# Kernel tuning notes

Hardware: AMD Instinct MI355X
Metric: run time of the kernel (lower is better)

## Reference

```python
import jax, jax.numpy as jnp
import numpy as np

NUM_HEADS = 8
LN_EPS = 1e-5


def _layernorm(x, g, b):
    m = jnp.mean(x, axis=-1, keepdims=True)
    v = jnp.mean(jnp.square(x - m), axis=-1, keepdims=True)
    return (x - m) * jax.lax.rsqrt(v + LN_EPS) * g + b


def setup_inputs() -> dict:
    key = jax.random.key(0)
    ks = jax.random.split(key, 10)
    D, C, Cin = 2, 256, 64  # depth, embed dim, input channels
    w = lambda k, shape: jax.random.normal(k, shape, jnp.float32) * 0.02
    return {
        "x": jax.random.normal(ks[0], (4, Cin, 12, 12, 12), jnp.float32),
        "W_pe": w(ks[1], (Cin, C)),
        "b_pe": jnp.zeros((C,), jnp.float32),
        "cls_token": w(ks[2], (1, 1, C)),
        "ln1_g": jnp.ones((D, C), jnp.float32),
        "ln1_b": jnp.zeros((D, C), jnp.float32),
        "Wqkv": w(ks[3], (D, C, 3 * C)),
        "Wproj": w(ks[4], (D, C, C)),
        "bproj": jnp.zeros((D, C), jnp.float32),
        "ln2_g": jnp.ones((D, C), jnp.float32),
        "ln2_b": jnp.zeros((D, C), jnp.float32),
        "W1": w(ks[5], (D, C, C)),
        "b1": jnp.zeros((D, C), jnp.float32),
        "W2": w(ks[6], (D, C, C)),
        "b2": jnp.zeros((D, C), jnp.float32),
        "normf_g": jnp.ones((C,), jnp.float32),
        "normf_b": jnp.zeros((C,), jnp.float32),
    }


def reference(x, W_pe, b_pe, cls_token, ln1_g, ln1_b, Wqkv, Wproj, bproj,
              ln2_g, ln2_b, W1, b1, W2, b2, normf_g, normf_b):
    B, Cin, H, W, L = x.shape
    C = W_pe.shape[1]
    hd = C // NUM_HEADS
    scale = hd ** (-0.5)

    # PatchEmbed: 1x1x1 Conv3d == per-voxel linear projection, then flatten to tokens
    tok = jnp.einsum('bchwl,cd->bhwld', x, W_pe).reshape(B, H * W * L, C) + b_pe
    cls = jnp.broadcast_to(cls_token, (B, 1, C))
    t = jnp.concatenate([cls, tok], axis=1)  # [B, N, C], N = H*W*L + 1
    N = t.shape[1]

    depth = Wqkv.shape[0]
    for i in range(depth):
        # --- self-attention ---
        y = _layernorm(t, ln1_g[i], ln1_b[i])
        qkv = (y @ Wqkv[i]).reshape(B, N, 3, NUM_HEADS, hd)
        qkv = jnp.transpose(qkv, (2, 0, 3, 1, 4))  # [3, B, H, N, hd]
        q, k, v = qkv[0], qkv[1], qkv[2]
        attn = jnp.einsum('bhnd,bhmd->bhnm', q, k) * scale
        attn = jax.nn.softmax(attn, axis=-1)
        o = jnp.einsum('bhnm,bhmd->bhnd', attn, v)
        o = jnp.transpose(o, (0, 2, 1, 3)).reshape(B, N, C)
        t = t + (o @ Wproj[i] + bproj[i])
        # --- MLP (mlp_ratio=1.0, exact GELU) ---
        y = _layernorm(t, ln2_g[i], ln2_b[i])
        h = jax.nn.gelu(y @ W1[i] + b1[i], approximate=False)
        t = t + (h @ W2[i] + b2[i])

    t = _layernorm(t, normf_g, normf_b)
    x_cls = t[:, 0]                                   # [B, C]
    feat = t[:, 1:]                                   # [B, H*W*L, C]
    feat = jnp.transpose(feat, (0, 2, 1)).reshape(B, C, H, W, L)  # downsample = Identity for dim=256
    return x_cls, feat
```

## Files before the change

### kernel.cpp

```cpp
#include <hip/hip_runtime.h>
#include <hip/hip_bf16.h>
#include <math.h>

#define B_   4
#define CIN  64
#define P_   1728
#define N_   1729
#define C_   256
#define NH_  8
#define HD_  32
#define M_   (B_*N_)
#define NPAD 1792

typedef __bf16 bf16x8 __attribute__((ext_vector_type(8)));
typedef __bf16 bf16x4 __attribute__((ext_vector_type(4)));
typedef float  f32x4  __attribute__((ext_vector_type(4)));

__global__ __launch_bounds__(256) void embed2(
    const float* __restrict__ x, const float* __restrict__ Wpe,
    const float* __restrict__ bpe, const float* __restrict__ cls,
    float* __restrict__ t)
{
    int idx = blockIdx.x*256 + threadIdx.x;
    int c   = idx & 255;
    int n   = (idx >> 8) % N_;
    int b   = idx / (N_*256);
    if (n == 0) { t[idx] = cls[c]; return; }
    int p = n - 1;
    float acc = bpe[c];
    for (int ci = 0; ci < CIN; ++ci)
        acc += x[(size_t)(b*CIN + ci)*P_ + p] * Wpe[ci*C_ + c];
    t[idx] = acc;
}

__global__ __launch_bounds__(256) void ln4(
    const float* __restrict__ in, __bf16* __restrict__ out,
    const float* __restrict__ g, const float* __restrict__ bb)
{
    int wv = threadIdx.x >> 6, lane = threadIdx.x & 63;
    size_t row = (size_t)blockIdx.x*4 + wv;
    float4 v = *(const float4*)&in[row*C_ + lane*4];
    float s1 = (v.x+v.y)+(v.z+v.w);
    float s2 = (v.x*v.x+v.y*v.y)+(v.z*v.z+v.w*v.w);
    #pragma unroll
    for (int off = 32; off >= 1; off >>= 1) {
        s1 += __shfl_xor(s1, off);
        s2 += __shfl_xor(s2, off);
    }
    float mean = s1*(1.0f/C_);
    float var  = fmaxf(s2*(1.0f/C_) - mean*mean, 0.0f);
    float rstd = rsqrtf(var + 1e-5f);
    float4 gg = *(const float4*)&g[lane*4];
    float4 bv = *(const float4*)&bb[lane*4];
    bf16x4 r;
    r[0] = (__bf16)((v.x-mean)*rstd*gg.x + bv.x);
    r[1] = (__bf16)((v.y-mean)*rstd*gg.y + bv.y);
    r[2] = (__bf16)((v.z-mean)*rstd*gg.z + bv.z);
    r[3] = (__bf16)((v.w-mean)*rstd*gg.w + bv.w);
    *(bf16x4*)&out[row*C_ + lane*4] = r;
}

__global__ __launch_bounds__(256) void ln4f(
    const float* __restrict__ in, float* __restrict__ out,
    const float* __restrict__ g, const float* __restrict__ bb,
    float* __restrict__ cls_out)
{
    int wv = threadIdx.x >> 6, lane = threadIdx.x & 63;
    size_t row = (size_t)blockIdx.x*4 + wv;
    float4 v = *(const float4*)&in[row*C_ + lane*4];
    float s1 = (v.x+v.y)+(v.z+v.w);
    float s2 = (v.x*v.x+v.y*v.y)+(v.z*v.z+v.w*v.w);
    #pragma unroll
    for (int off = 32; off >= 1; off >>= 1) {
        s1 += __shfl_xor(s1, off);
        s2 += __shfl_xor(s2, off);
    }
    float mean = s1*(1.0f/C_);
    float var  = fmaxf(s2*(1.0f/C_) - mean*mean, 0.0f);
    float rstd = rsqrtf(var + 1e-5f);
    float4 gg = *(const float4*)&g[lane*4];
    float4 bv = *(const float4*)&bb[lane*4];
    float4 r;
    r.x = (v.x-mean)*rstd*gg.x + bv.x;
    r.y = (v.y-mean)*rstd*gg.y + bv.y;
    r.z = (v.z-mean)*rstd*gg.z + bv.z;
    r.w = (v.w-mean)*rstd*gg.w + bv.w;
    *(float4*)&out[row*C_ + lane*4] = r;
    if ((row % N_) == 0)
        *(float4*)&cls_out[(row / N_)*C_ + lane*4] = r;
}

__global__ __launch_bounds__(256) void wprep2(
    const float* __restrict__ Wqkv, const float* __restrict__ Wproj,
    const float* __restrict__ W1,   const float* __restrict__ W2,
    __bf16* __restrict__ wT)
{
    int z = blockIdx.z, which = z >> 1, layer = z & 1;
    const float* src; __bf16* dst; int NC;
    if (which == 0) {
        src = Wqkv + (size_t)layer*C_*768;
        dst = wT   + (size_t)layer*768*256;
        NC  = 768;
    } else {
        NC = 256;
        const float* b3 = (which == 1) ? Wproj : (which == 2) ? W1 : W2;
        src = b3 + (size_t)layer*65536;
        dst = wT + 2*768*256 + (size_t)((which-1)*2 + layer)*65536;
    }
    int n0 = blockIdx.x*32; if (n0 >= NC) return;
    int k0 = blockIdx.y*32;
    __shared__ float tile[32][33];
    int c = threadIdx.x & 31, r = threadIdx.x >> 5;
    for (int rr = r; rr < 32; rr += 8)
        tile[rr][c] = src[(size_t)(k0+rr)*NC + n0 + c];
    __syncthreads();
    for (int rr = r; rr < 32; rr += 8)
        dst[(size_t)(n0+rr)*256 + k0 + c] = (__bf16)tile[c][rr];
}

__global__ __launch_bounds__(256) void padzero(
    __bf16* __restrict__ kB, __bf16* __restrict__ vB)
{
    int idx = blockIdx.x*256 + threadIdx.x;
    if (idx >= 32*63*32) return;
    int d  = idx & 31;
    int n  = (idx >> 5) % 63 + N_;
    int bh = idx / (63*32);
    kB[((size_t)bh*NPAD + n)*32 + d] = (__bf16)0.f;
    vB[((size_t)bh*32 + d)*NPAD + n] = (__bf16)0.f;
}

template<int NC, bool ADD, bool GELU, bool BIAS, bool OUTBF>
__global__ __launch_bounds__(256) void gemm3(
    const __bf16* __restrict__ A, const __bf16* __restrict__ Wt,
    const float* __restrict__ bias, float* __restrict__ outF,
    __bf16* __restrict__ outB)
{
    __shared__ __align__(16) __bf16 As[64*64];
    __shared__ __align__(16) __bf16 Bs[64*64];
    int r0 = blockIdx.x*64, c0 = blockIdx.y*64;
    int tid = threadIdx.x;
    int wv = tid >> 6, lane = tid & 63, quad = lane >> 4, mn = lane & 15;
    int sr = tid >> 2, sc = tid & 3;
    int ga = r0 + sr; if (ga >= M_) ga = M_ - 1;

    f32x4 acc[4];
    #pragma unroll
    for (int ct = 0; ct < 4; ++ct)
        #pragma unroll
        for (int rr = 0; rr < 4; ++rr) acc[ct][rr] = 0.f;

    for (int kc = 0; kc < 4; ++kc) {
        __syncthreads();
        *(bf16x8*)&As[sr*64 + ((sc ^ (sr & 7))*8)] =
            *(const bf16x8*)&A[(size_t)ga*256 + kc*64 + sc*8];
        *(bf16x8*)&As[sr*64 + (((sc+4) ^ (sr & 7))*8)] =
            *(const bf16x8*)&A[(size_t)ga*256 + kc*64 + sc*8 + 32];
        *(bf16x8*)&Bs[sr*64 + ((sc ^ (sr & 7))*8)] =
            *(const bf16x8*)&Wt[(size_t)(c0+sr)*256 + kc*64 + sc*8];
        *(bf16x8*)&Bs[sr*64 + (((sc+4) ^ (sr & 7))*8)] =
            *(const bf16x8*)&Wt[(size_t)(c0+sr)*256 + kc*64 + sc*8 + 32];
        __syncthreads();

        #pragma unroll
        for (int h = 0; h < 2; ++h) {
            bf16x8 a = *(const bf16x8*)&As[(wv*16 + mn)*64 + (((h*4+quad) ^ (mn & 7))*8)];
            #pragma unroll
            for (int ct = 0; ct < 4; ++ct) {
                bf16x8 b = *(const bf16x8*)&Bs[(ct*16 + mn)*64 + (((h*4+quad) ^ (mn & 7))*8)];
                acc[ct] = __builtin_amdgcn_mfma_f32_16x16x32_bf16(a, b, acc[ct], 0, 0, 0);
            }
        }
    }

    #pragma unroll
    for (int ct = 0; ct < 4; ++ct) {
        int col = c0 + ct*16 + mn;
        #pragma unroll
        for (int rr = 0; rr < 4; ++rr) {
            int row = r0 + wv*16 + quad*4 + rr;
            if (row >= M_) continue;
            float val = acc[ct][rr];
            if (BIAS) val += bias[col];
            if (GELU) val = 0.5f*val*(1.f + erff(val*0.70710678118654752f));
            size_t oi = (size_t)row*NC + col;
            if (OUTBF) outB[oi] = (__bf16)val;
            else if (ADD) outF[oi] += val;
            else outF[oi] = val;
        }
    }
}

__global__ __launch_bounds__(256) void gemm_qkv3(
    const __bf16* __restrict__ A, const __bf16* __restrict__ Wt,
    __bf16* __restrict__ qB, __bf16* __restrict__ kB, __bf16* __restrict__ vB)
{
    __shared__ __align__(16) __bf16 As[64*64];
    __shared__ __align__(16) __bf16 Bs[64*64];
    int r0 = blockIdx.x*64, c0 = blockIdx.y*64;
    int tid = threadIdx.x;
    int wv = tid >> 6, lane = tid & 63, quad = lane >> 4, mn = lane & 15;
    int sr = tid >> 2, sc = tid & 3;
    int ga = r0 + sr; if (ga >= M_) ga = M_ - 1;

    f32x4 acc[4];
    #pragma unroll
    for (int ct = 0; ct < 4; ++ct)
        #pragma unroll
        for (int rr = 0; rr < 4; ++rr) acc[ct][rr] = 0.f;

    for (int kc = 0; kc < 4; ++kc) {
        __syncthreads();
        *(bf16x8*)&As[sr*64 + ((sc ^ (sr & 7))*8)] =
            *(const bf16x8*)&A[(size_t)ga*256 + kc*64 + sc*8];
        *(bf16x8*)&As[sr*64 + (((sc+4) ^ (sr & 7))*8)] =
            *(const bf16x8*)&A[(size_t)ga*256 + kc*64 + sc*8 + 32];
        *(bf16x8*)&Bs[sr*64 + ((sc ^ (sr & 7))*8)] =
            *(const bf16x8*)&Wt[(size_t)(c0+sr)*256 + kc*64 + sc*8];
        *(bf16x8*)&Bs[sr*64 + (((sc+4) ^ (sr & 7))*8)] =
            *(const bf16x8*)&Wt[(size_t)(c0+sr)*256 + kc*64 + sc*8 + 32];
        __syncthreads();

        #pragma unroll
        for (int h = 0; h < 2; ++h) {
            bf16x8 a = *(const bf16x8*)&As[(wv*16 + mn)*64 + (((h*4+quad) ^ (mn & 7))*8)];
            #pragma unroll
            for (int ct = 0; ct < 4; ++ct) {
                bf16x8 b = *(const bf16x8*)&Bs[(ct*16 + mn)*64 + (((h*4+quad) ^ (mn & 7))*8)];
                acc[ct] = __builtin_amdgcn_mfma_f32_16x16x32_bf16(a, b, acc[ct], 0, 0, 0);
            }
        }
    }

    const float scale = 0.17677669529663687f;
    #pragma unroll
    for (int ct = 0; ct < 4; ++ct) {
        int col = c0 + ct*16 + mn;
        #pragma unroll
        for (int rr = 0; rr < 4; ++rr) {
            int row = r0 + wv*16 + quad*4 + rr;
            if (row >= M_) continue;
            int b = row / N_, n = row - b*N_;
            float val = acc[ct][rr];
            if (col < 256) {
                int h = col >> 5, dd = col & 31;
                qB[((size_t)(b*NH_+h)*NPAD + n)*32 + dd] = (__bf16)(val*scale);
            } else if (col < 512) {
                int h = (col-256) >> 5, dd = col & 31;
                kB[((size_t)(b*NH_+h)*NPAD + n)*32 + dd] = (__bf16)val;
            } else {
                int h = (col-512) >> 5, dd = col & 31;
                vB[((size_t)(b*NH_+h)*32 + dd)*NPAD + n] = (__bf16)val;
            }
        }
    }
}

__global__ __launch_bounds__(256) void attn11(
    const __bf16* __restrict__ qB, const __bf16* __restrict__ kB,
    const __bf16* __restrict__ vB, __bf16* __restrict__ o)
{
    int bh = blockIdx.x, b = bh >> 3, h = bh & 7;
    int q0 = blockIdx.y * 64;
    int tid = threadIdx.x;
    int wv = tid >> 6, lane = tid & 63, quad = lane >> 4, mn = lane & 15;

    __shared__ __align__(16) __bf16 lk[128*32];
    __shared__ __align__(16) __bf16 lvt[32*128];
    __shared__ __align__(16) __bf16 lp[4][16*72];

    bf16x8 qfrag = *(const bf16x8*)(
        qB + ((size_t)bh*NPAD + q0 + wv*16 + mn)*32 + quad*8);

    f32x4 oacc0, oacc1;
    #pragma unroll
    for (int rr = 0; rr < 4; ++rr) { oacc0[rr]=0.f; oacc1[rr]=0.f; }
    float lsum = 0.f;

    const __bf16* kbase = kB + (size_t)bh*NPAD*32;
    const __bf16* vbase = vB + (size_t)bh*32*NPAD;
    int sr = tid >> 2, sc = tid & 3;
    int vr = tid >> 3, vc = tid & 7;

    for (int t = 0; t < 14; ++t) {
        int k0 = t*128;
        __syncthreads();
        #pragma unroll
        for (int hh = 0; hh < 2; ++hh) {
            int r = hh*64 + sr;
            *(bf16x8*)&lk[r*32 + ((sc ^ (r & 3))*8)] =
                *(const bf16x8*)(kbase + (size_t)(k0 + r)*32 + sc*8);
            int cp = hh*8 + vc;
            *(bf16x8*)&lvt[vr*128 + ((cp ^ (vr & 7))*8)] =
                *(const bf16x8*)(vbase + (size_t)vr*NPAD + k0 + cp*8);
        }
        __syncthreads();

        #pragma unroll
        for (int h2 = 0; h2 < 2; ++h2) {
            #pragma unroll
            for (int ct = 0; ct < 4; ++ct) {
                int kr = h2*64 + ct*16 + mn;
                bf16x8 kf = *(const bf16x8*)&lk[kr*32 + ((quad ^ (mn & 3))*8)];
                f32x4 z;
                #pragma unroll
                for (int rr = 0; rr < 4; ++rr) z[rr] = 0.f;
                f32x4 st = __builtin_amdgcn_mfma_f32_16x16x32_bf16(kf, qfrag, z, 0, 0, 0);

                bf16x4 pf4;
                #pragma unroll
                for (int rr = 0; rr < 4; ++rr) {
                    float p = __expf(st[rr]);
                    pf4[rr] = (__bf16)p;
                    lsum += p;
                }
                *(bf16x4*)&lp[wv][mn*72 + ct*16 + quad*4] = pf4;
            }

            #pragma unroll
            for (int kh = 0; kh < 2; ++kh) {
                bf16x8 pf = *(const bf16x8*)&lp[wv][mn*72 + kh*32 + quad*8];
                int chunk = h2*8 + kh*4 + quad;
                int vsw = (chunk ^ (mn & 7)) * 8;
                bf16x8 v0 = *(const bf16x8*)&lvt[ mn      *128 + vsw];
                bf16x8 v1 = *(const bf16x8*)&lvt[(mn+16)*128 + vsw];
                oacc0 = __builtin_amdgcn_mfma_f32_16x16x32_bf16(pf, v0, oacc0, 0, 0, 0);
                oacc1 = __builtin_amdgcn_mfma_f32_16x16x32_bf16(pf, v1, oacc1, 0, 0, 0);
            }
        }
    }

    lsum += __shfl_xor(lsum, 16);
    lsum += __shfl_xor(lsum, 32);
    lsum -= 63.0f;

    #pragma unroll
    for (int rr = 0; rr < 4; ++rr) {
        float l = __shfl(lsum, quad*4 + rr);
        int q = q0 + wv*16 + quad*4 + rr;
        if (q >= N_) continue;
        float inv = 1.0f / l;
        size_t base = ((size_t)(b*N_ + q))*C_ + h*HD_;
        o[base + mn]      = (__bf16)(oacc0[rr]*inv);
        o[base + 16 + mn] = (__bf16)(oacc1[rr]*inv);
    }
}

__global__ __launch_bounds__(256) void feat3(
    const float* __restrict__ y, float* __restrict__ outf)
{
    __shared__ float tl[32][33];
    int p0 = blockIdx.x*32, c0 = blockIdx.y*32, b = blockIdx.z;
    int cc = threadIdx.x & 31, rr = threadIdx.x >> 5;
    for (int i = rr; i < 32; i += 8)
        tl[i][cc] = y[((size_t)(b*N_) + 1 + p0 + i)*C_ + c0 + cc];
    __syncthreads();
    for (int i = rr; i < 32; i += 8)
        outf[((size_t)(b*C_) + c0 + i)*P_ + p0 + cc] = tl[cc][i];
}

extern "C" void kernel_launch(void* const* d_in, const int* in_sizes, int n_in,
                              void* d_out, int out_size, void* d_ws, size_t ws_size,
                              hipStream_t stream)
{
    const float* x        = (const float*)d_in[0];
    const float* W_pe     = (const float*)d_in[1];
    const float* b_pe     = (const float*)d_in[2];
    const float* cls_tok  = (const float*)d_in[3];
    const float* ln1_g    = (const float*)d_in[4];
    const float* ln1_b    = (const float*)d_in[5];
    const float* Wqkv     = (const float*)d_in[6];
    const float* Wproj    = (const float*)d_in[7];
    const float* bproj    = (const float*)d_in[8];
    const float* ln2_g    = (const float*)d_in[9];
    const float* ln2_b    = (const float*)d_in[10];
    const float* W1       = (const float*)d_in[11];
    const float* b1       = (const float*)d_in[12];
    const float* W2       = (const float*)d_in[13];
    const float* b2       = (const float*)d_in[14];
    const float* normf_g  = (const float*)d_in[15];
    const float* normf_b  = (const float*)d_in[16];

    const size_t MC = (size_t)M_*C_;
    float*  ws  = (float*)d_ws;
    float*  t   = ws;
    float*  yf  = ws + MC;
    __bf16* ybf = (__bf16*)(ws + 2*MC);
    __bf16* hbf = (__bf16*)(ws + 2*MC + MC/2);
    __bf16* obf = (__bf16*)(ws + 2*MC + MC);
    __bf16* wT  = (__bf16*)(ws + 2*MC + 3*(MC/2));
    __bf16* qB  = wT + 2*768*256 + 6*256*256;
    __bf16* kB  = qB + (size_t)B_*NH_*NPAD*32;
    __bf16* vB  = kB + (size_t)B_*NH_*NPAD*32;

    __bf16* projT = wT + 2*768*256;
    __bf16* w1T   = projT + 2*256*256;
    __bf16* w2T   = w1T   + 2*256*256;

    float* out_cls  = (float*)d_out;
    float* out_feat = out_cls + B_*C_;

    wprep2<<<dim3(24, 8, 8), 256, 0, stream>>>(Wqkv, Wproj, W1, W2, wT);
    padzero<<<252, 256, 0, stream>>>(kB, vB);
    embed2<<<(B_*N_*C_)/256, 256, 0, stream>>>(x, W_pe, b_pe, cls_tok, t);

    const int GRID_M = (M_ + 63) / 64;
    for (int i = 0; i < 2; ++i) {
        ln4<<<M_/4, 256, 0, stream>>>(t, ybf, ln1_g + i*C_, ln1_b + i*C_);
        gemm_qkv3<<<dim3(GRID_M, 12), 256, 0, stream>>>(
            ybf, wT + (size_t)i*768*256, qB, kB, vB);
        attn11<<<dim3(32, 28), 256, 0, stream>>>(qB, kB, vB, obf);
        gemm3<256,true,false,true,false><<<dim3(GRID_M, 4), 256, 0, stream>>>(
            obf, projT + (size_t)i*65536, bproj + i*C_, t, nullptr);
        ln4<<<M_/4, 256, 0, stream>>>(t, ybf, ln2_g + i*C_, ln2_b + i*C_);
        gemm3<256,false,true,true,true><<<dim3(GRID_M, 4), 256, 0, stream>>>(
            ybf, w1T + (size_t)i*65536, b1 + i*C_, nullptr, hbf);
        gemm3<256,true,false,true,false><<<dim3(GRID_M, 4), 256, 0, stream>>>(
            hbf, w2T + (size_t)i*65536, b2 + i*C_, t, nullptr);
    }

    ln4f<<<M_/4, 256, 0, stream>>>(t, yf, normf_g, normf_b, out_cls);
    feat3<<<dim3(54, 8, 4), 256, 0, stream>>>(yf, out_feat);
}
```

Measured before the change: 293.4 us.

## Split attention over key dimension into two halves with a combine kernel

Attention now runs as two blocks per query tile, each covering half of the keys (7 of 14 tiles). Each block writes unnormalized partial outputs and row sums, and a new combine kernel adds the halves and normalizes. The aim is to double the attention grid so the GPU fills better. The price is an extra launch and extra global traffic for the bf16 partials. The softmax exponent also moves to exp2f, with log2(e) folded into the q scale. Both the no-max softmax and the -63 padding correction are kept as before.

```diff
diff --git a/kernel.cpp b/kernel.cpp
--- a/kernel.cpp
+++ b/kernel.cpp
@@ -232,7 +232,7 @@
         }
     }
 
-    const float scale = 0.17677669529663687f;
+    const float scale = 0.25503473109f;
     #pragma unroll
     for (int ct = 0; ct < 4; ++ct) {
         int col = c0 + ct*16 + mn;
@@ -256,12 +256,14 @@
     }
 }
 
-__global__ __launch_bounds__(256) void attn11(
+__global__ __launch_bounds__(256) void attn12(
     const __bf16* __restrict__ qB, const __bf16* __restrict__ kB,
-    const __bf16* __restrict__ vB, __bf16* __restrict__ o)
-{
-    int bh = blockIdx.x, b = bh >> 3, h = bh & 7;
+    const __bf16* __restrict__ vB, __bf16* __restrict__ oP,
+    float* __restrict__ lP)
+{
+    int bh = blockIdx.x;
     int q0 = blockIdx.y * 64;
+    int half = blockIdx.z;
     int tid = threadIdx.x;
     int wv = tid >> 6, lane = tid & 63, quad = lane >> 4, mn = lane & 15;
 
@@ -282,8 +284,8 @@
     int sr = tid >> 2, sc = tid & 3;
     int vr = tid >> 3, vc = tid & 7;
 
-    for (int t = 0; t < 14; ++t) {
-        int k0 = t*128;
+    for (int t = 0; t < 7; ++t) {
+        int k0 = half*896 + t*128;
         __syncthreads();
         #pragma unroll
         for (int hh = 0; hh < 2; ++hh) {
@@ -310,7 +312,7 @@
                 bf16x4 pf4;
                 #pragma unroll
                 for (int rr = 0; rr < 4; ++rr) {
-                    float p = __expf(st[rr]);
+                    float p = exp2f(st[rr]);
                     pf4[rr] = (__bf16)p;
                     lsum += p;
                 }
@@ -332,18 +334,37 @@
 
     lsum += __shfl_xor(lsum, 16);
     lsum += __shfl_xor(lsum, 32);
-    lsum -= 63.0f;
+    if (quad == 0)
+        lP[((size_t)(half*32 + bh))*NPAD + q0 + wv*16 + mn] = lsum;
 
     #pragma unroll
     for (int rr = 0; rr < 4; ++rr) {
-        float l = __shfl(lsum, quad*4 + rr);
         int q = q0 + wv*16 + quad*4 + rr;
-        if (q >= N_) continue;
-        float inv = 1.0f / l;
-        size_t base = ((size_t)(b*N_ + q))*C_ + h*HD_;
-        o[base + mn]      = (__bf16)(oacc0[rr]*inv);
-        o[base + 16 + mn] = (__bf16)(oacc1[rr]*inv);
-    }
+        size_t base = (((size_t)(half*32 + bh))*NPAD + q)*32;
+        oP[base + mn]      = (__bf16)oacc0[rr];
+        oP[base + 16 + mn] = (__bf16)oacc1[rr];
+    }
+}
+
+__global__ __launch_bounds__(256) void attn_comb(
+    const __bf16* __restrict__ oP, const float* __restrict__ lP,
+    __bf16* __restrict__ o)
+{
+    int idx = blockIdx.x*256 + threadIdx.x;
+    int d4 = idx & 7;
+    int q  = (idx >> 3) % NPAD;
+    int bh = idx / (NPAD*8);
+    if (q >= N_) return;
+    int b = bh >> 3, h = bh & 7;
+    float l = lP[(size_t)bh*NPAD + q] + lP[((size_t)(32 + bh))*NPAD + q] - 63.0f;
+    float inv = 1.0f / l;
+    bf16x4 o1 = *(const bf16x4*)&oP[(((size_t)bh)*NPAD + q)*32 + d4*4];
+    bf16x4 o2 = *(const bf16x4*)&oP[(((size_t)(32 + bh))*NPAD + q)*32 + d4*4];
+    bf16x4 r;
+    #pragma unroll
+    for (int j = 0; j < 4; ++j)
+        r[j] = (__bf16)(((float)o1[j] + (float)o2[j]) * inv);
+    *(bf16x4*)&o[((size_t)(b*N_ + q))*C_ + h*HD_ + d4*4] = r;
 }
 
 __global__ __launch_bounds__(256) void feat3(
@@ -392,6 +413,8 @@
     __bf16* qB  = wT + 2*768*256 + 6*256*256;
     __bf16* kB  = qB + (size_t)B_*NH_*NPAD*32;
     __bf16* vB  = kB + (size_t)B_*NH_*NPAD*32;
+    __bf16* oP  = vB + (size_t)B_*NH_*NPAD*32;
+    float*  lP  = (float*)(oP + (size_t)2*B_*NH_*NPAD*32);
 
     __bf16* projT = wT + 2*768*256;
     __bf16* w1T   = projT + 2*256*256;
@@ -409,7 +432,8 @@
         ln4<<<M_/4, 256, 0, stream>>>(t, ybf, ln1_g + i*C_, ln1_b + i*C_);
         gemm_qkv3<<<dim3(GRID_M, 12), 256, 0, stream>>>(
             ybf, wT + (size_t)i*768*256, qB, kB, vB);
-        attn11<<<dim3(32, 28), 256, 0, stream>>>(qB, kB, vB, obf);
+        attn12<<<dim3(32, 28, 2), 256, 0, stream>>>(qB, kB, vB, oP, lP);
+        attn_comb<<<(32*NPAD*8)/256, 256, 0, stream>>>(oP, lP, obf);
         gemm3<256,true,false,true,false><<<dim3(GRID_M, 4), 256, 0, stream>>>(
             obf, projT + (size_t)i*65536, bproj + i*C_, t, nullptr);
         ln4<<<M_/4, 256, 0, stream>>>(t, ybf, ln2_g + i*C_, ln2_b + i*C_);
```

New measurement: 306.3 us. 1.04x slower.
